# Kernel tuning notes

Measured on AMD Instinct MI355X. Metric: run time of the kernel, lower is better.

## Reference

```python
import jax, jax.numpy as jnp
import numpy as np

N = 50000      # nodes
E = 1600000    # edges
F_IN = 8       # node_features
H = 64         # hidden_dim
P = 5          # poly_degree
L = 3          # n_layers


def setup_inputs() -> dict:
    key = jax.random.key(0)
    ks = jax.random.split(key, 20)
    s = lambda *shape: 0.05
    inp = {
        "x": jax.random.normal(ks[0], (N, F_IN), jnp.float32),
        "edge_index": jax.random.randint(ks[1], (2, E), 0, N, jnp.int32),
        "edge_weight": jax.random.uniform(ks[2], (E,), jnp.float32),
        # input projection (xavier-ish)
        "W_in": jax.random.normal(ks[3], (H, F_IN), jnp.float32) * 0.15,
        "b_in": jnp.zeros((H,), jnp.float32),
        # per-layer coeff_net: Linear(H+4 -> 32) -> ReLU -> Linear(32 -> P+1) -> Softmax
        "coeff_W1": jax.random.normal(ks[4], (L, 32, H + 4), jnp.float32) * 0.1,
        "coeff_b1": jnp.zeros((L, 32), jnp.float32),
        "coeff_W2": jax.random.normal(ks[5], (L, P + 1, 32), jnp.float32) * 0.1,
        "coeff_b2": jnp.zeros((L, P + 1), jnp.float32),
        # per-layer LayerNorm params
        "ln_scale": jnp.ones((L, H), jnp.float32),
        "ln_bias": jnp.zeros((L, H), jnp.float32),
        # edge predictor: Linear(2H->H) ReLU Linear(H->H//2) ReLU Linear(H//2->1) Sigmoid
        "ep_W1": jax.random.normal(ks[6], (H, 2 * H), jnp.float32) * 0.08,
        "ep_b1": jnp.zeros((H,), jnp.float32),
        "ep_W2": jax.random.normal(ks[7], (H // 2, H), jnp.float32) * 0.1,
        "ep_b2": jnp.zeros((H // 2,), jnp.float32),
        "ep_W3": jax.random.normal(ks[8], (1, H // 2), jnp.float32) * 0.15,
        "ep_b3": jnp.zeros((1,), jnp.float32),
    }
    return inp


def _layernorm(v, scale, bias, eps=1e-5):
    m = v.mean(-1, keepdims=True)
    var = v.var(-1, keepdims=True)
    return (v - m) / jnp.sqrt(var + eps) * scale + bias


def _diffusion(h, row, col, norm, cW1, cb1, cW2, cb2):
    # coefficient MLP conditioned on graph stats (std is unbiased, as torch)
    x_mean = h.mean(0)
    stats = jnp.stack([h.mean(), h.std(ddof=1),
                       jnp.float32(N), jnp.float32(E)])
    ci = jnp.concatenate([x_mean, stats])           # (H+4,)
    hid = jax.nn.relu(ci @ cW1.T + cb1)             # (32,)
    coeffs = jax.nn.softmax(hid @ cW2.T + cb2)      # (P+1,)
    result = coeffs[0] * h
    tx = h
    for k in range(1, P + 1):
        msg = norm[:, None] * tx[col]               # (E, H) gather + scale
        tx = jax.ops.segment_sum(msg, row, num_segments=N)  # scatter-add SpMM
        result = result + coeffs[k] * tx
    return result


def reference(x, edge_index, edge_weight,
              W_in, b_in,
              coeff_W1, coeff_b1, coeff_W2, coeff_b2,
              ln_scale, ln_bias,
              ep_W1, ep_b1, ep_W2, ep_b2, ep_W3, ep_b3):
    row, col = edge_index[0], edge_index[1]
    # symmetric normalization T = D^{-1/2} A D^{-1/2} (identical every layer)
    deg = jnp.zeros((N,), x.dtype).at[col].add(edge_weight)
    dis = jnp.minimum(deg ** -0.5, 1e6)             # clamp(max=1e6) caps inf
    dis = jnp.where(jnp.isinf(dis), 0.0, dis)
    norm = dis[row] * edge_weight * dis[col]        # (E,)

    h = x @ W_in.T + b_in                           # (N, H)
    for l in range(L):
        h_new = _diffusion(h, row, col, norm,
                           coeff_W1[l], coeff_b1[l], coeff_W2[l], coeff_b2[l])
        h = _layernorm(h + h_new, ln_scale[l], ln_bias[l])

    ef = jnp.concatenate([h[row], h[col]], axis=-1)             # (E, 2H)
    e1 = jax.nn.relu(ef @ ep_W1.T + ep_b1)
    e2 = jax.nn.relu(e1 @ ep_W2.T + ep_b2)
    edge_preds = jax.nn.sigmoid(e2 @ ep_W3.T + ep_b3)[:, 0]     # (E,)
    return edge_preds, h
```

## Files before the change

### kernel.cpp

```cpp
#include <hip/hip_runtime.h>
#include <hip/hip_bf16.h>
#include <hip/hip_fp16.h>

typedef __hip_bfloat16 bf16;
typedef __attribute__((ext_vector_type(8))) short short8;
typedef __attribute__((ext_vector_type(8))) _Float16 half8;
typedef __attribute__((ext_vector_type(2))) _Float16 half2v;
typedef __attribute__((ext_vector_type(4))) float f32x4;

#define N_NODES 50000
#define N_EDGES 1600000
#define FIN 8
#define HD 64
#define NH (N_NODES * HD)
#define NLAYERS 3

#define RSLC 256
#define EPR (N_EDGES / RSLC)
#define NWORDS 12500
#define DSLC2 128
#define EPD2 (N_EDGES / DSLC2)
#define DWORDS 25000
#define DEGSCALE 512.0f

__device__ __forceinline__ float b2f(bf16 v) { return __bfloat162float(v); }
__device__ __forceinline__ float bu2f(unsigned int u) { return __uint_as_float(u << 16); }
__device__ __forceinline__ unsigned short f2bu(float f) {
    unsigned int x = __float_as_uint(f);
    unsigned int r = x + 0x7FFFu + ((x >> 16) & 1u);
    return (unsigned short)(r >> 16);
}
__device__ __forceinline__ unsigned short f2h(float f) {
    _Float16 h = (_Float16)f;
    return *(unsigned short*)&h;
}
union H16 { unsigned short b; _Float16 h; };
__device__ __forceinline__ float h16f(unsigned u) {
    H16 x; x.b = (unsigned short)u;
    return (float)x.h;
}

__global__ void k_detect(const void* __restrict__ ew, int* __restrict__ flag) {
    int ok = 1;
    for (int i = threadIdx.x; i < 512; i += 64) {
        float v = b2f(((const bf16*)ew)[i]);
        if (!(v >= 0.f && v <= 1.f)) ok = 0;
    }
    unsigned long long m = __ballot(ok);
    if (threadIdx.x == 0) *flag = (m == 0xFFFFFFFFFFFFFFFFull) ? 0 : 1;
}

struct ConvArgs {
    const void* src[14];
    float* dst[14];
    int cum[15];
};

__global__ void k_conv_small(ConvArgs a, const int* __restrict__ flag) {
    int q = blockIdx.x * 256 + threadIdx.x;
    if (q >= a.cum[14]) return;
    int s = 0;
    while (q >= a.cum[s + 1]) ++s;
    int off = q - a.cum[s];
    if (*flag) a.dst[s][off] = ((const float*)a.src[s])[off];
    else       a.dst[s][off] = bu2f(((const unsigned short*)a.src[s])[off]);
}

__global__ void k_w1h(const float* __restrict__ W1, unsigned short* __restrict__ w1h) {
    int i = blockIdx.x * 256 + threadIdx.x;
    if (i >= 8192) return;
    int r = i >> 6, k = i & 63;
    float v = (r < 64) ? W1[r * 128 + k] : W1[(r - 64) * 128 + 64 + k];
    w1h[i] = f2h(v);
}

__global__ void __launch_bounds__(1024) k_deg2(const int* __restrict__ ei,
                                               const void* __restrict__ ewr,
                                               const int* __restrict__ flag,
                                               unsigned short* __restrict__ pdeg16) {
    __shared__ unsigned int sm[DWORDS];
    int b = blockIdx.x, t = threadIdx.x;
    for (int i = t; i < DWORDS; i += 1024) sm[i] = 0;
    __syncthreads();
    int f32 = *flag;
    int ebase = b * EPD2;
    for (int el = t; el < EPD2; el += 1024) {
        int e = ebase + el;
        int c = ei[N_EDGES + e];
        float w = f32 ? ((const float*)ewr)[e] : bu2f(((const unsigned short*)ewr)[e]);
        unsigned fx = (unsigned)__float2int_rn(w * DEGSCALE);
        atomicAdd(&sm[c >> 1], fx << ((c & 1) * 16));
    }
    __syncthreads();
    unsigned int* dst = (unsigned int*)(pdeg16 + (size_t)b * N_NODES);
    for (int i = t; i < DWORDS; i += 1024) dst[i] = sm[i];
}

__global__ void k_dis(const unsigned short* __restrict__ pdeg16,
                      float* __restrict__ dis, float* __restrict__ dis2) {
    int n = blockIdx.x * 256 + threadIdx.x;
    if (n >= N_NODES) return;
    unsigned s = 0;
#pragma unroll 8
    for (int k = 0; k < DSLC2; ++k) s += pdeg16[(size_t)k * N_NODES + n];
    float d = (float)s * (1.f / DEGSCALE);
    float di = fminf(rsqrtf(d), 1e6f);
    dis[n] = di;
    dis2[n] = di * di;
}


__global__ void __launch_bounds__(1024) k_hist_row(const int* __restrict__ ei,
                                                   unsigned int* __restrict__ pcnt_u32) {
    __shared__ unsigned int sm[NWORDS];
    int b = blockIdx.x, t = threadIdx.x;
    for (int i = t; i < NWORDS; i += 1024) sm[i] = 0;
    __syncthreads();
    int ebase = b * EPR;
    for (int el = t; el < EPR; el += 1024) {
        int r = ei[ebase + el];
        atomicAdd(&sm[r >> 2], 1u << ((r & 3) * 8));
    }
    __syncthreads();
    unsigned int* dst = pcnt_u32 + (size_t)b * NWORDS;
    for (int i = t; i < NWORDS; i += 1024) dst[i] = sm[i];
}

__global__ void k_merge(const unsigned char* __restrict__ pcnt8,
                        int* __restrict__ cnt,
                        unsigned short* __restrict__ pref16, int* __restrict__ bsum) {
    __shared__ int red[256];
    int t = threadIdx.x;
    int n = blockIdx.x * 256 + t;
    int run = 0;
    if (n < N_NODES) {
#pragma unroll 8
        for (int s = 0; s < RSLC; ++s) {
            pref16[(size_t)s * N_NODES + n] = (unsigned short)run;
            run += pcnt8[(size_t)s * N_NODES + n];
        }
        cnt[n] = run;
    }
    red[t] = run;
    __syncthreads();
    for (int off = 128; off; off >>= 1) {
        if (t < off) red[t] += red[t + off];
        __syncthreads();
    }
    if (t == 0) bsum[blockIdx.x] = red[0];
}

__global__ void k_scan_top(const int* __restrict__ bsum, int* __restrict__ bpre,
                           int* __restrict__ row_ptr) {
    __shared__ int sm[256];
    int t = threadIdx.x;
    int v = (t < 196) ? bsum[t] : 0;
    sm[t] = v;
    __syncthreads();
    int val = v;
    for (int off = 1; off < 256; off <<= 1) {
        int other = (t >= off) ? sm[t - off] : 0;
        __syncthreads();
        val += other;
        sm[t] = val;
        __syncthreads();
    }
    bpre[t] = val - v;
    if (t == 0) row_ptr[N_NODES] = N_EDGES;
}

__global__ void k_scan_fin(const int* __restrict__ cnt, const int* __restrict__ bpre,
                           int* __restrict__ row_ptr) {
    __shared__ int sm[256];
    int t = threadIdx.x;
    int n = blockIdx.x * 256 + t;
    int v = (n < N_NODES) ? cnt[n] : 0;
    sm[t] = v;
    __syncthreads();
    int val = v;
    for (int off = 1; off < 256; off <<= 1) {
        int other = (t >= off) ? sm[t - off] : 0;
        __syncthreads();
        val += other;
        sm[t] = val;
        __syncthreads();
    }
    if (n < N_NODES) row_ptr[n] = bpre[blockIdx.x] + val - v;
}

__global__ void __launch_bounds__(1024) k_placeA(const int* __restrict__ ei,
                                                 const void* __restrict__ ewr,
                                                 const int* __restrict__ flag,
                                                 const int* __restrict__ row_ptr,
                                                 const unsigned short* __restrict__ pref16,
                                                 unsigned int* __restrict__ pairs4,
                                                 int* __restrict__ iperm) {
    __shared__ unsigned int sm[NWORDS];
    int b = blockIdx.x, t = threadIdx.x;
    for (int i = t; i < NWORDS; i += 1024) sm[i] = 0;
    __syncthreads();
    int f32 = *flag;
    int ebase = b * EPR;
    const unsigned short* pr = pref16 + (size_t)b * N_NODES;
    for (int el = t; el < EPR; el += 1024) {
        int e = ebase + el;
        int r = ei[e];
        int c = ei[N_EDGES + e];
        float w = f32 ? ((const float*)ewr)[e] : bu2f(((const unsigned short*)ewr)[e]);
        int sh = (r & 3) * 8;
        unsigned old = atomicAdd(&sm[r >> 2], 1u << sh);
        int ord = (old >> sh) & 0xFF;
        int pos = row_ptr[r] + pr[r] + ord;
        pairs4[pos] = ((unsigned)c << 16) | (unsigned)f2h(w);
        iperm[e] = pos;
    }
}

__global__ void __launch_bounds__(256) k_rc(const int* __restrict__ row_ptr,
                                            const unsigned int* __restrict__ pairs4,
                                            unsigned int* __restrict__ rc) {
    int lane = threadIdx.x & 63;
    int wv = __builtin_amdgcn_readfirstlane((int)(blockIdx.x * 4 + (threadIdx.x >> 6)));
    int s = __builtin_amdgcn_readfirstlane(row_ptr[wv]);
    int e = __builtin_amdgcn_readfirstlane(row_ptr[wv + 1]);
    unsigned rhi = ((unsigned)wv) << 16;
    for (int pos = s + lane; pos < e; pos += 64)
        rc[pos] = (pairs4[pos] >> 16) | rhi;
}


__global__ void k_inproj(const void* __restrict__ xr_, const float* __restrict__ W,
                         const float* __restrict__ b, const float* __restrict__ dis,
                         float* __restrict__ h,
                         unsigned short* __restrict__ h_bf, const int* __restrict__ flag) {
    __shared__ float Wt[FIN * HD];
    __shared__ float bs[HD];
    int t = threadIdx.x;
    int f32 = *flag;
    for (int idx = t; idx < FIN * HD; idx += 256) {
        int f = idx >> 3, j = idx & 7;
        Wt[j * 64 + f] = W[idx];
    }
    if (t < 64) bs[t] = b[t];
    __syncthreads();
    int gid = blockIdx.x * 256 + t;
    if (gid < NH) {
        int i = gid >> 6, f = gid & 63;
        const float* xf = (const float*)xr_ + i * FIN;
        const unsigned short* xb = (const unsigned short*)xr_ + i * FIN;
        float acc = bs[f];
#pragma unroll
        for (int j = 0; j < FIN; ++j) {
            float xv = f32 ? xf[j] : bu2f(xb[j]);
            acc += xv * Wt[j * 64 + f];
        }
        h[gid] = acc;
        h_bf[gid] = f2bu(acc * dis[i]);
    }
}


__global__ void k_stats(const float* __restrict__ h, float* __restrict__ stats) {
    __shared__ float ssum[256], ssq[256];
    int t = threadIdx.x;
    float ls = 0.f, lq = 0.f;
    for (int idx = blockIdx.x * 256 + t; idx < NH; idx += 102400) {
        float v = h[idx];
        ls += v; lq += v * v;
    }
    ssum[t] = ls; ssq[t] = lq;
    __syncthreads();
    if (t < 64) {
        float a = ssum[t] + ssum[t + 64] + ssum[t + 128] + ssum[t + 192];
        atomicAdd(&stats[t], a);
        float q = ssq[t] + ssq[t + 64] + ssq[t + 128] + ssq[t + 192];
        for (int off = 32; off; off >>= 1) q += __shfl_down(q, off, 64);
        if (t == 0) atomicAdd(&stats[64], q);
    }
}

__global__ void k_coeffs(const float* __restrict__ stats,
                         const float* __restrict__ W1, const float* __restrict__ b1,
                         const float* __restrict__ W2, const float* __restrict__ b2,
                         int layer, float* __restrict__ coeffs) {
    __shared__ float ci[68];
    __shared__ float hid[32];
    __shared__ float lg[6];
    int t = threadIdx.x;
    float sf = stats[t];
    float tot = sf;
    for (int off = 1; off < 64; off <<= 1) tot += __shfl_xor(tot, off, 64);
    ci[t] = sf / (float)N_NODES;
    if (t == 0) {
        float sumsq = stats[64];
        float mean = tot / (float)NH;
        float var = (sumsq - (float)NH * mean * mean) / (float)(NH - 1);
        ci[64] = mean;
        ci[65] = sqrtf(fmaxf(var, 0.f));
        ci[66] = (float)N_NODES;
        ci[67] = (float)N_EDGES;
    }
    __syncthreads();
    if (t < 32) {
        float a = b1[layer * 32 + t];
        const float* wr = W1 + (layer * 32 + t) * 68;
        for (int j = 0; j < 68; ++j) a += ci[j] * wr[j];
        hid[t] = fmaxf(a, 0.f);
    }
    __syncthreads();
    if (t < 6) {
        float a = b2[layer * 6 + t];
        const float* wr = W2 + (layer * 6 + t) * 32;
        for (int g = 0; g < 32; ++g) a += hid[g] * wr[g];
        lg[t] = a;
    }
    __syncthreads();
    if (t == 0) {
        float mx = lg[0];
        for (int p = 1; p < 6; ++p) mx = fmaxf(mx, lg[p]);
        float s = 0.f, e[6];
        for (int p = 0; p < 6; ++p) { e[p] = expf(lg[p] - mx); s += e[p]; }
        for (int p = 0; p < 6; ++p) coeffs[p] = e[p] / s;
    }
}


__device__ __forceinline__ float acc_range(const unsigned short* __restrict__ txo,
                                           const unsigned int* __restrict__ pairs4,
                                           int j0, int j1, int lane, float acc) {
    int j = j0;
    for (; j + 15 < j1; j += 16) {
        unsigned p0 = pairs4[j],      p1 = pairs4[j + 1],  p2 = pairs4[j + 2],  p3 = pairs4[j + 3];
        unsigned p4 = pairs4[j + 4],  p5 = pairs4[j + 5],  p6 = pairs4[j + 6],  p7 = pairs4[j + 7];
        unsigned p8 = pairs4[j + 8],  p9 = pairs4[j + 9],  pa = pairs4[j + 10], pb = pairs4[j + 11];
        unsigned pc = pairs4[j + 12], pd = pairs4[j + 13], pe = pairs4[j + 14], pf = pairs4[j + 15];
        float g0 = bu2f(txo[(p0 >> 16) * 64 + lane]);
        float g1 = bu2f(txo[(p1 >> 16) * 64 + lane]);
        float g2 = bu2f(txo[(p2 >> 16) * 64 + lane]);
        float g3 = bu2f(txo[(p3 >> 16) * 64 + lane]);
        float g4 = bu2f(txo[(p4 >> 16) * 64 + lane]);
        float g5 = bu2f(txo[(p5 >> 16) * 64 + lane]);
        float g6 = bu2f(txo[(p6 >> 16) * 64 + lane]);
        float g7 = bu2f(txo[(p7 >> 16) * 64 + lane]);
        float g8 = bu2f(txo[(p8 >> 16) * 64 + lane]);
        float g9 = bu2f(txo[(p9 >> 16) * 64 + lane]);
        float ga = bu2f(txo[(pa >> 16) * 64 + lane]);
        float gb = bu2f(txo[(pb >> 16) * 64 + lane]);
        float gc = bu2f(txo[(pc >> 16) * 64 + lane]);
        float gd = bu2f(txo[(pd >> 16) * 64 + lane]);
        float ge = bu2f(txo[(pe >> 16) * 64 + lane]);
        float gf = bu2f(txo[(pf >> 16) * 64 + lane]);
        acc += h16f(p0) * g0 + h16f(p1) * g1 + h16f(p2) * g2 + h16f(p3) * g3;
        acc += h16f(p4) * g4 + h16f(p5) * g5 + h16f(p6) * g6 + h16f(p7) * g7;
        acc += h16f(p8) * g8 + h16f(p9) * g9 + h16f(pa) * ga + h16f(pb) * gb;
        acc += h16f(pc) * gc + h16f(pd) * gd + h16f(pe) * ge + h16f(pf) * gf;
    }
    for (; j + 7 < j1; j += 8) {
        unsigned p0 = pairs4[j],     p1 = pairs4[j + 1], p2 = pairs4[j + 2], p3 = pairs4[j + 3];
        unsigned p4 = pairs4[j + 4], p5 = pairs4[j + 5], p6 = pairs4[j + 6], p7 = pairs4[j + 7];
        float g0 = bu2f(txo[(p0 >> 16) * 64 + lane]);
        float g1 = bu2f(txo[(p1 >> 16) * 64 + lane]);
        float g2 = bu2f(txo[(p2 >> 16) * 64 + lane]);
        float g3 = bu2f(txo[(p3 >> 16) * 64 + lane]);
        float g4 = bu2f(txo[(p4 >> 16) * 64 + lane]);
        float g5 = bu2f(txo[(p5 >> 16) * 64 + lane]);
        float g6 = bu2f(txo[(p6 >> 16) * 64 + lane]);
        float g7 = bu2f(txo[(p7 >> 16) * 64 + lane]);
        acc += h16f(p0) * g0 + h16f(p1) * g1 + h16f(p2) * g2 + h16f(p3) * g3;
        acc += h16f(p4) * g4 + h16f(p5) * g5 + h16f(p6) * g6 + h16f(p7) * g7;
    }
    for (; j < j1; ++j) {
        unsigned p = pairs4[j];
        acc += h16f(p) * bu2f(txo[(p >> 16) * 64 + lane]);
    }
    return acc;
}

__global__ void __launch_bounds__(256) k_spmm(
    const unsigned short* __restrict__ txo, unsigned short* __restrict__ txn,
    const int* __restrict__ row_ptr, const unsigned int* __restrict__ pairs4,
    const float* __restrict__ dis2) {
    int lane = threadIdx.x & 63;
    int wv = __builtin_amdgcn_readfirstlane((int)(blockIdx.x * 4 + (threadIdx.x >> 6)));
    int s = __builtin_amdgcn_readfirstlane(row_ptr[wv]);
    int e = __builtin_amdgcn_readfirstlane(row_ptr[wv + 1]);
    float acc = acc_range(txo, pairs4, s, e, lane, 0.f);
    float d2 = dis2[wv];
    txn[wv * 64 + lane] = f2bu(acc * d2);
}


__global__ void __launch_bounds__(256) k_spmm_ln(
    const unsigned short* __restrict__ txo,
    const int* __restrict__ row_ptr, const unsigned int* __restrict__ pairs4,
    float* __restrict__ h, unsigned short* __restrict__ h_bf,
    const unsigned short* __restrict__ t1, const unsigned short* __restrict__ t2,
    const unsigned short* __restrict__ t3, const unsigned short* __restrict__ t4,
    const float* __restrict__ coeffs, const float* __restrict__ dis,
    const float* __restrict__ sc, const float* __restrict__ bi,
    int layer, int last, void* __restrict__ outv, const int* __restrict__ flag) {
    int lane = threadIdx.x & 63;
    int wv = __builtin_amdgcn_readfirstlane((int)(blockIdx.x * 4 + (threadIdx.x >> 6)));
    int s = __builtin_amdgcn_readfirstlane(row_ptr[wv]);
    int e = __builtin_amdgcn_readfirstlane(row_ptr[wv + 1]);
    float acc = acc_range(txo, pairs4, s, e, lane, 0.f);
    int o = wv * 64 + lane;
    float ds = dis[wv];
    float invd = 1.f / ds;
    float c0 = coeffs[0], c1 = coeffs[1], c2 = coeffs[2],
          c3 = coeffs[3], c4 = coeffs[4], c5 = coeffs[5];
    float v = (1.f + c0) * h[o] +
              invd * (c1 * bu2f(t1[o]) + c2 * bu2f(t2[o]) +
                      c3 * bu2f(t3[o]) + c4 * bu2f(t4[o])) +
              c5 * ds * acc;
    float m = v;
    for (int off = 1; off < 64; off <<= 1) m += __shfl_xor(m, off, 64);
    m *= (1.f / 64.f);
    float d = v - m;
    float q = d * d;
    for (int off = 1; off < 64; off <<= 1) q += __shfl_xor(q, off, 64);
    float var = q * (1.f / 64.f);
    float y = d / sqrtf(var + 1e-5f) * sc[layer * 64 + lane] + bi[layer * 64 + lane];
    h[o] = y;
    h_bf[o] = f2bu(y * ds);
    if (last) {
        if (*flag) ((float*)outv)[N_EDGES + o] = y;
        else       ((unsigned short*)outv)[N_EDGES + o] = f2bu(y);
    }
}

union U4H8 { uint4 u; half8 h; };

__global__ void __launch_bounds__(256) k_uv(const float* __restrict__ h,
                                            const unsigned short* __restrict__ w1h,
                                            unsigned short* __restrict__ ub,
                                            unsigned short* __restrict__ vb) {
    int t = threadIdx.x;
    int lane = t & 63;
    int m = lane & 15, q = lane >> 4;
    int wv = blockIdx.x * 4 + (t >> 6);
    if (wv >= N_NODES / 16) return;
    int node0 = wv * 16;
    const float* hrow = h + (size_t)(node0 + m) * 64 + q * 8;
    U4H8 a0, a1;
#pragma unroll
    for (int j = 0; j < 8; ++j) a0.h[j] = (_Float16)hrow[j];
#pragma unroll
    for (int j = 0; j < 8; ++j) a1.h[j] = (_Float16)hrow[32 + j];
#pragma unroll
    for (int ct = 0; ct < 8; ++ct) {
        const unsigned short* wrow = w1h + (size_t)(ct * 16 + m) * 64 + q * 8;
        U4H8 b0, b1;
        b0.u = *(const uint4*)wrow;
        b1.u = *(const uint4*)(wrow + 32);
        f32x4 acc = {0.f, 0.f, 0.f, 0.f};
        acc = __builtin_amdgcn_mfma_f32_16x16x32_f16(a0.h, b0.h, acc, 0, 0, 0);
        acc = __builtin_amdgcn_mfma_f32_16x16x32_f16(a1.h, b1.h, acc, 0, 0, 0);
        int feat = ct * 16 + m;
        unsigned short* dst = (feat < 64) ? (ub + feat) : (vb + (feat - 64));
#pragma unroll
        for (int r = 0; r < 4; ++r) {
            int node = node0 + q * 4 + r;
            dst[(size_t)node * 64] = f2h(acc[r]);
        }
    }
}

__device__ __forceinline__ unsigned h2rel(unsigned uu, unsigned vv, half2v b) {
    half2v a = *(half2v*)&uu + *(half2v*)&vv + b;
    a[0] = a[0] > (_Float16)0 ? a[0] : (_Float16)0;
    a[1] = a[1] > (_Float16)0 ? a[1] : (_Float16)0;
    return *(unsigned*)&a;
}

__global__ void __launch_bounds__(256) k_edgepred(
    const unsigned short* __restrict__ ub, const unsigned short* __restrict__ vb,
    const unsigned int* __restrict__ rc,
    const float* __restrict__ eb1, const float* __restrict__ eW2,
    const float* __restrict__ eb2, const float* __restrict__ eW3,
    const float* __restrict__ eb3, float* __restrict__ tmpP) {
    int t = threadIdx.x;
    int lane = t & 63;
    int m = lane & 15, q = lane >> 4;

    half8 B00, B01, B10, B11;
#pragma unroll
    for (int j = 0; j < 8; ++j) {
        B00[j] = (_Float16)eW2[(m) * 64      + q * 8 + j];
        B01[j] = (_Float16)eW2[(m) * 64 + 32 + q * 8 + j];
        B10[j] = (_Float16)eW2[(m + 16) * 64      + q * 8 + j];
        B11[j] = (_Float16)eW2[(m + 16) * 64 + 32 + q * 8 + j];
    }
    half2v b1p0[4], b1p1[4];
#pragma unroll
    for (int wq = 0; wq < 4; ++wq) {
        b1p0[wq][0] = (_Float16)eb1[q * 8 + 2 * wq];
        b1p0[wq][1] = (_Float16)eb1[q * 8 + 2 * wq + 1];
        b1p1[wq][0] = (_Float16)eb1[32 + q * 8 + 2 * wq];
        b1p1[wq][1] = (_Float16)eb1[32 + q * 8 + 2 * wq + 1];
    }
    float w3a = eW3[m], w3b = eW3[16 + m];
    float b2a = eb2[m], b2b = eb2[16 + m];
    float b3v = eb3[0];

    int gw = blockIdx.x * 4 + (t >> 6);
    const int NW = 2500 * 4;
    for (int tp = gw; tp < N_EDGES / 32; tp += NW) {
        int base0 = (tp * 2) << 4;
        int base1 = base0 + 16;
        unsigned rcv0 = rc[base0 + m];
        unsigned rcv1 = rc[base1 + m];
        const unsigned short* up0 = ub + (rcv0 >> 16) * 64;
        const unsigned short* vp0 = vb + (rcv0 & 0xFFFFu) * 64;
        const unsigned short* up1 = ub + (rcv1 >> 16) * 64;
        const unsigned short* vp1 = vb + (rcv1 & 0xFFFFu) * 64;
        uint4 U00 = *(const uint4*)(up0 + q * 8);
        uint4 U01 = *(const uint4*)(up0 + 32 + q * 8);
        uint4 V00 = *(const uint4*)(vp0 + q * 8);
        uint4 V01 = *(const uint4*)(vp0 + 32 + q * 8);
        uint4 U10 = *(const uint4*)(up1 + q * 8);
        uint4 U11 = *(const uint4*)(up1 + 32 + q * 8);
        uint4 V10 = *(const uint4*)(vp1 + q * 8);
        uint4 V11 = *(const uint4*)(vp1 + 32 + q * 8);

        U4H8 a0, a1;
        a0.u.x = h2rel(U00.x, V00.x, b1p0[0]);
        a0.u.y = h2rel(U00.y, V00.y, b1p0[1]);
        a0.u.z = h2rel(U00.z, V00.z, b1p0[2]);
        a0.u.w = h2rel(U00.w, V00.w, b1p0[3]);
        a1.u.x = h2rel(U01.x, V01.x, b1p1[0]);
        a1.u.y = h2rel(U01.y, V01.y, b1p1[1]);
        a1.u.z = h2rel(U01.z, V01.z, b1p1[2]);
        a1.u.w = h2rel(U01.w, V01.w, b1p1[3]);
        f32x4 acc0 = {0.f, 0.f, 0.f, 0.f};
        f32x4 acc1 = {0.f, 0.f, 0.f, 0.f};
        acc0 = __builtin_amdgcn_mfma_f32_16x16x32_f16(a0.h, B00, acc0, 0, 0, 0);
        acc0 = __builtin_amdgcn_mfma_f32_16x16x32_f16(a1.h, B01, acc0, 0, 0, 0);
        acc1 = __builtin_amdgcn_mfma_f32_16x16x32_f16(a0.h, B10, acc1, 0, 0, 0);
        acc1 = __builtin_amdgcn_mfma_f32_16x16x32_f16(a1.h, B11, acc1, 0, 0, 0);
        float z0[4];
#pragma unroll
        for (int rr = 0; rr < 4; ++rr) {
            z0[rr] = w3a * fmaxf(acc0[rr] + b2a, 0.f) + w3b * fmaxf(acc1[rr] + b2b, 0.f);
            z0[rr] += __shfl_xor(z0[rr], 1, 64);
            z0[rr] += __shfl_xor(z0[rr], 2, 64);
            z0[rr] += __shfl_xor(z0[rr], 4, 64);
            z0[rr] += __shfl_xor(z0[rr], 8, 64);
        }

        U4H8 c0, c1;
        c0.u.x = h2rel(U10.x, V10.x, b1p0[0]);
        c0.u.y = h2rel(U10.y, V10.y, b1p0[1]);
        c0.u.z = h2rel(U10.z, V10.z, b1p0[2]);
        c0.u.w = h2rel(U10.w, V10.w, b1p0[3]);
        c1.u.x = h2rel(U11.x, V11.x, b1p1[0]);
        c1.u.y = h2rel(U11.y, V11.y, b1p1[1]);
        c1.u.z = h2rel(U11.z, V11.z, b1p1[2]);
        c1.u.w = h2rel(U11.w, V11.w, b1p1[3]);
        f32x4 acc2 = {0.f, 0.f, 0.f, 0.f};
        f32x4 acc3 = {0.f, 0.f, 0.f, 0.f};
        acc2 = __builtin_amdgcn_mfma_f32_16x16x32_f16(c0.h, B00, acc2, 0, 0, 0);
        acc2 = __builtin_amdgcn_mfma_f32_16x16x32_f16(c1.h, B01, acc2, 0, 0, 0);
        acc3 = __builtin_amdgcn_mfma_f32_16x16x32_f16(c0.h, B10, acc3, 0, 0, 0);
        acc3 = __builtin_amdgcn_mfma_f32_16x16x32_f16(c1.h, B11, acc3, 0, 0, 0);
        float z1[4];
#pragma unroll
        for (int rr = 0; rr < 4; ++rr) {
            z1[rr] = w3a * fmaxf(acc2[rr] + b2a, 0.f) + w3b * fmaxf(acc3[rr] + b2b, 0.f);
            z1[rr] += __shfl_xor(z1[rr], 1, 64);
            z1[rr] += __shfl_xor(z1[rr], 2, 64);
            z1[rr] += __shfl_xor(z1[rr], 4, 64);
            z1[rr] += __shfl_xor(z1[rr], 8, 64);
        }

        if (m == 0) {
#pragma unroll
            for (int rr = 0; rr < 4; ++rr) {
                float p0 = 1.f / (1.f + __expf(-(z0[rr] + b3v)));
                float p1 = 1.f / (1.f + __expf(-(z1[rr] + b3v)));
                tmpP[base0 + (q << 2) + rr] = p0;
                tmpP[base1 + (q << 2) + rr] = p1;
            }
        }
    }
}

__global__ void k_out(const int* __restrict__ iperm, const float* __restrict__ tmpP,
                      void* __restrict__ outv, const int* __restrict__ flag) {
    int e = blockIdx.x * 256 + threadIdx.x;
    if (e >= N_EDGES) return;
    float p = tmpP[iperm[e]];
    if (*flag) ((float*)outv)[e] = p;
    else       ((unsigned short*)outv)[e] = f2bu(p);
}


extern "C" void kernel_launch(void* const* d_in, const int* in_sizes, int n_in,
                              void* d_out, int out_size, void* d_ws, size_t ws_size,
                              hipStream_t stream) {
    (void)in_sizes; (void)n_in; (void)out_size; (void)ws_size;
    const void* x_r   = d_in[0];
    const int*  ei    = (const int*)d_in[1];
    const void* ew_r  = d_in[2];

    char* w = (char*)d_ws;
    float* h            = (float*)w;          w += (size_t)NH * 4;
    unsigned short* hbf = (unsigned short*)w; w += (size_t)NH * 2;
    char* txr           = w;                  w += (size_t)NH * 8;
    unsigned int* pairs4 = (unsigned int*)w;  w += (size_t)N_EDGES * 4;
    unsigned int* rc    = (unsigned int*)w;   w += (size_t)N_EDGES * 4;
    int* iperm          = (int*)w;            w += (size_t)N_EDGES * 4;
    int* row_ptr        = (int*)w;            w += 200192;
    int* cnt            = (int*)w;            w += 200192;
    float* dis          = (float*)w;          w += 200192;
    float* dis2         = (float*)w;          w += 200192;
    float* cWin = (float*)w; w += 2048;
    float* cbin = (float*)w; w += 256;
    float* ccW1 = (float*)w; w += 26112;
    float* ccb1 = (float*)w; w += 384;
    float* ccW2 = (float*)w; w += 2304;
    float* ccb2 = (float*)w; w += 128;
    float* clns = (float*)w; w += 768;
    float* clnb = (float*)w; w += 768;
    float* ceW1 = (float*)w; w += 32768;
    float* ceb1 = (float*)w; w += 256;
    float* ceW2 = (float*)w; w += 8192;
    float* ceb2 = (float*)w; w += 128;
    float* ceW3 = (float*)w; w += 128;
    float* ceb3 = (float*)w; w += 128;
    unsigned short* w1h = (unsigned short*)w; w += 16384;
    int* bsum = (int*)w; w += 1024;
    int* bpre = (int*)w; w += 1024;
    char* zero_base = w;
    float* stats = (float*)w; w += 1024;
    size_t zero_bytes = (size_t)(w - zero_base);
    float* coeffs = (float*)w; w += 128;
    int*   flag   = (int*)w;   w += 128;

    unsigned int* pcnt_u32 = (unsigned int*)pairs4;
    unsigned char* pcnt8   = (unsigned char*)pairs4;
    unsigned short* pref16 = (unsigned short*)txr;
    unsigned short* pdeg16 = (unsigned short*)h;
    float* tmpP            = (float*)pairs4;

    unsigned short* tx[4];
    for (int k = 0; k < 4; ++k) tx[k] = (unsigned short*)txr + (size_t)k * NH;
    unsigned short* ub = tx[0];
    unsigned short* vb = tx[1];

    (void)hipMemsetAsync(zero_base, 0, zero_bytes, stream);

    k_detect<<<1, 64, 0, stream>>>(ew_r, flag);

    ConvArgs ca;
    const void* srcs[14] = {d_in[3], d_in[4], d_in[5], d_in[6], d_in[7], d_in[8], d_in[9],
                            d_in[10], d_in[11], d_in[12], d_in[13], d_in[14], d_in[15], d_in[16]};
    float* dsts[14] = {cWin, cbin, ccW1, ccb1, ccW2, ccb2, clns,
                       clnb, ceW1, ceb1, ceW2, ceb2, ceW3, ceb3};
    int sizes[14] = {512, 64, 6528, 96, 576, 18, 192, 192, 8192, 64, 2048, 32, 32, 1};
    int c = 0;
    for (int i = 0; i < 14; ++i) { ca.src[i] = srcs[i]; ca.dst[i] = dsts[i]; ca.cum[i] = c; c += sizes[i]; }
    ca.cum[14] = c;
    k_conv_small<<<(c + 255) / 256, 256, 0, stream>>>(ca, flag);
    k_w1h<<<32, 256, 0, stream>>>(ceW1, w1h);

    k_deg2<<<DSLC2, 1024, 0, stream>>>(ei, ew_r, flag, pdeg16);
    k_hist_row<<<RSLC, 1024, 0, stream>>>(ei, pcnt_u32);
    k_merge<<<196, 256, 0, stream>>>(pcnt8, cnt, pref16, bsum);
    k_scan_top<<<1, 256, 0, stream>>>(bsum, bpre, row_ptr);
    k_scan_fin<<<196, 256, 0, stream>>>(cnt, bpre, row_ptr);
    k_placeA<<<RSLC, 1024, 0, stream>>>(ei, ew_r, flag, row_ptr, pref16, pairs4, iperm);
    k_rc<<<12500, 256, 0, stream>>>(row_ptr, pairs4, rc);
    k_dis<<<196, 256, 0, stream>>>(pdeg16, dis, dis2);
    k_inproj<<<12500, 256, 0, stream>>>(x_r, cWin, cbin, dis, h, hbf, flag);

    for (int l = 0; l < NLAYERS; ++l) {
        k_stats<<<400, 256, 0, stream>>>(h, stats + l * 80);
        k_coeffs<<<1, 64, 0, stream>>>(stats + l * 80, ccW1, ccb1, ccW2, ccb2, l,
                                       coeffs + l * 8);
        const unsigned short* src = hbf;
        for (int k = 0; k < 4; ++k) {
            k_spmm<<<12500, 256, 0, stream>>>(src, tx[k], row_ptr, pairs4, dis2);
            src = tx[k];
        }
        k_spmm_ln<<<12500, 256, 0, stream>>>(tx[3], row_ptr, pairs4, h, hbf,
                                             tx[0], tx[1], tx[2], tx[3],
                                             coeffs + l * 8, dis, clns, clnb, l,
                                             (l == NLAYERS - 1) ? 1 : 0, d_out, flag);
    }

    k_uv<<<782, 256, 0, stream>>>(h, w1h, ub, vb);
    k_edgepred<<<2500, 256, 0, stream>>>(ub, vb, rc, ceb1, ceW2, ceb2, ceW3, ceb3, tmpP);
    k_out<<<6250, 256, 0, stream>>>(iperm, tmpP, d_out, flag);
}
```

Measured before the change: 796.0 us.

## Fuse row histogram with degree accumulation and fold dis into merge

Combines the row-count histogram and the weighted in-degree accumulation into one kernel. Each 1024-thread block now holds both LDS histograms and reads its slice of edge_index once, not in two separate passes. The inverse-sqrt degree computation moves into the merge kernel, removing a launch. Degree partials now use 256 slices instead of 128, which doubles the partial-sum buffer the merge must read and needs about 150KB of LDS per block. The edge-predictor grid is also cut from 2500 to 2048 blocks, and iperm moves earlier in the workspace.

```diff
diff --git a/kernel.cpp b/kernel.cpp
--- a/kernel.cpp
+++ b/kernel.cpp
@@ -18,8 +18,6 @@
 #define RSLC 256
 #define EPR (N_EDGES / RSLC)
 #define NWORDS 12500
-#define DSLC2 128
-#define EPD2 (N_EDGES / DSLC2)
 #define DWORDS 25000
 #define DEGSCALE 512.0f
 
@@ -74,60 +72,39 @@
     w1h[i] = f2h(v);
 }
 
-__global__ void __launch_bounds__(1024) k_deg2(const int* __restrict__ ei,
-                                               const void* __restrict__ ewr,
-                                               const int* __restrict__ flag,
-                                               unsigned short* __restrict__ pdeg16) {
-    __shared__ unsigned int sm[DWORDS];
+__global__ void __launch_bounds__(1024) k_histdeg2(const int* __restrict__ ei,
+                                                   const void* __restrict__ ewr,
+                                                   const int* __restrict__ flag,
+                                                   unsigned int* __restrict__ pcnt_u32,
+                                                   unsigned short* __restrict__ pdeg16) {
+    __shared__ unsigned int sm_h[NWORDS];
+    __shared__ unsigned int sm_d[DWORDS];
     int b = blockIdx.x, t = threadIdx.x;
-    for (int i = t; i < DWORDS; i += 1024) sm[i] = 0;
+    for (int i = t; i < NWORDS; i += 1024) sm_h[i] = 0;
+    for (int i = t; i < DWORDS; i += 1024) sm_d[i] = 0;
     __syncthreads();
     int f32 = *flag;
-    int ebase = b * EPD2;
-    for (int el = t; el < EPD2; el += 1024) {
+    int ebase = b * EPR;
+    for (int el = t; el < EPR; el += 1024) {
         int e = ebase + el;
+        int r = ei[e];
+        atomicAdd(&sm_h[r >> 2], 1u << ((r & 3) * 8));
         int c = ei[N_EDGES + e];
         float w = f32 ? ((const float*)ewr)[e] : bu2f(((const unsigned short*)ewr)[e]);
         unsigned fx = (unsigned)__float2int_rn(w * DEGSCALE);
-        atomicAdd(&sm[c >> 1], fx << ((c & 1) * 16));
-    }
-    __syncthreads();
-    unsigned int* dst = (unsigned int*)(pdeg16 + (size_t)b * N_NODES);
-    for (int i = t; i < DWORDS; i += 1024) dst[i] = sm[i];
-}
-
-__global__ void k_dis(const unsigned short* __restrict__ pdeg16,
-                      float* __restrict__ dis, float* __restrict__ dis2) {
-    int n = blockIdx.x * 256 + threadIdx.x;
-    if (n >= N_NODES) return;
-    unsigned s = 0;
-#pragma unroll 8
-    for (int k = 0; k < DSLC2; ++k) s += pdeg16[(size_t)k * N_NODES + n];
-    float d = (float)s * (1.f / DEGSCALE);
-    float di = fminf(rsqrtf(d), 1e6f);
-    dis[n] = di;
-    dis2[n] = di * di;
-}
-
-
-__global__ void __launch_bounds__(1024) k_hist_row(const int* __restrict__ ei,
-                                                   unsigned int* __restrict__ pcnt_u32) {
-    __shared__ unsigned int sm[NWORDS];
-    int b = blockIdx.x, t = threadIdx.x;
-    for (int i = t; i < NWORDS; i += 1024) sm[i] = 0;
-    __syncthreads();
-    int ebase = b * EPR;
-    for (int el = t; el < EPR; el += 1024) {
-        int r = ei[ebase + el];
-        atomicAdd(&sm[r >> 2], 1u << ((r & 3) * 8));
-    }
-    __syncthreads();
-    unsigned int* dst = pcnt_u32 + (size_t)b * NWORDS;
-    for (int i = t; i < NWORDS; i += 1024) dst[i] = sm[i];
+        atomicAdd(&sm_d[c >> 1], fx << ((c & 1) * 16));
+    }
+    __syncthreads();
+    unsigned int* dsth = pcnt_u32 + (size_t)b * NWORDS;
+    for (int i = t; i < NWORDS; i += 1024) dsth[i] = sm_h[i];
+    unsigned int* dstd = (unsigned int*)(pdeg16 + (size_t)b * N_NODES);
+    for (int i = t; i < DWORDS; i += 1024) dstd[i] = sm_d[i];
 }
 
 __global__ void k_merge(const unsigned char* __restrict__ pcnt8,
-                        int* __restrict__ cnt,
+                        const unsigned short* __restrict__ pdeg16,
+                        int* __restrict__ cnt, float* __restrict__ dis,
+                        float* __restrict__ dis2,
                         unsigned short* __restrict__ pref16, int* __restrict__ bsum) {
     __shared__ int red[256];
     int t = threadIdx.x;
@@ -140,6 +117,13 @@
             run += pcnt8[(size_t)s * N_NODES + n];
         }
         cnt[n] = run;
+        unsigned s = 0;
+#pragma unroll 8
+        for (int k = 0; k < RSLC; ++k) s += pdeg16[(size_t)k * N_NODES + n];
+        float d = (float)s * (1.f / DEGSCALE);
+        float di = fminf(rsqrtf(d), 1e6f);
+        dis[n] = di;
+        dis2[n] = di * di;
     }
     red[t] = run;
     __syncthreads();
@@ -504,7 +488,7 @@
     float b3v = eb3[0];
 
     int gw = blockIdx.x * 4 + (t >> 6);
-    const int NW = 2500 * 4;
+    const int NW = 2048 * 4;
     for (int tp = gw; tp < N_EDGES / 32; tp += NW) {
         int base0 = (tp * 2) << 4;
         int base1 = base0 + 16;
@@ -606,10 +590,10 @@
     char* w = (char*)d_ws;
     float* h            = (float*)w;          w += (size_t)NH * 4;
     unsigned short* hbf = (unsigned short*)w; w += (size_t)NH * 2;
+    int* iperm          = (int*)w;            w += (size_t)N_EDGES * 4;
     char* txr           = w;                  w += (size_t)NH * 8;
     unsigned int* pairs4 = (unsigned int*)w;  w += (size_t)N_EDGES * 4;
     unsigned int* rc    = (unsigned int*)w;   w += (size_t)N_EDGES * 4;
-    int* iperm          = (int*)w;            w += (size_t)N_EDGES * 4;
     int* row_ptr        = (int*)w;            w += 200192;
     int* cnt            = (int*)w;            w += 200192;
     float* dis          = (float*)w;          w += 200192;
@@ -664,14 +648,12 @@
     k_conv_small<<<(c + 255) / 256, 256, 0, stream>>>(ca, flag);
     k_w1h<<<32, 256, 0, stream>>>(ceW1, w1h);
 
-    k_deg2<<<DSLC2, 1024, 0, stream>>>(ei, ew_r, flag, pdeg16);
-    k_hist_row<<<RSLC, 1024, 0, stream>>>(ei, pcnt_u32);
-    k_merge<<<196, 256, 0, stream>>>(pcnt8, cnt, pref16, bsum);
+    k_histdeg2<<<RSLC, 1024, 0, stream>>>(ei, ew_r, flag, pcnt_u32, pdeg16);
+    k_merge<<<196, 256, 0, stream>>>(pcnt8, pdeg16, cnt, dis, dis2, pref16, bsum);
     k_scan_top<<<1, 256, 0, stream>>>(bsum, bpre, row_ptr);
     k_scan_fin<<<196, 256, 0, stream>>>(cnt, bpre, row_ptr);
     k_placeA<<<RSLC, 1024, 0, stream>>>(ei, ew_r, flag, row_ptr, pref16, pairs4, iperm);
     k_rc<<<12500, 256, 0, stream>>>(row_ptr, pairs4, rc);
-    k_dis<<<196, 256, 0, stream>>>(pdeg16, dis, dis2);
     k_inproj<<<12500, 256, 0, stream>>>(x_r, cWin, cbin, dis, h, hbf, flag);
 
     for (int l = 0; l < NLAYERS; ++l) {
@@ -690,6 +672,6 @@
     }
 
     k_uv<<<782, 256, 0, stream>>>(h, w1h, ub, vb);
-    k_edgepred<<<2500, 256, 0, stream>>>(ub, vb, rc, ceb1, ceW2, ceb2, ceW3, ceb3, tmpP);
+    k_edgepred<<<2048, 256, 0, stream>>>(ub, vb, rc, ceb1, ceW2, ceb2, ceW3, ceb3, tmpP);
     k_out<<<6250, 256, 0, stream>>>(iperm, tmpP, d_out, flag);
 }
```

Result: no change. 792.0 us (-0.5%).
